# Kernel tuning notes

Measured on AMD Instinct MI355X. Metric: run time of the kernel, lower is better.

## Reference

```python
import jax, jax.numpy as jnp
import numpy as np

B, S, H, E, V, EXTRA = 256, 400, 512, 512, 50257, 100
EMB = H + E  # embedding_size


def setup_inputs() -> dict:
    key = jax.random.key(0)
    ks = jax.random.split(key, 20)
    sd = lambda *shape: 1.0 / np.sqrt(shape[-1])
    d = {
        "input_step": jax.random.normal(ks[0], (B, EMB), jnp.float32),
        "last_hidden": jax.random.normal(ks[1], (1, B, H), jnp.float32),
        "encoder_outputs": jax.random.normal(ks[2], (S, B, H), jnp.float32),
        "enc_batch_extend_vocab": jax.random.randint(ks[3], (S, B), 0, V + EXTRA, jnp.int32),
        "extra_zeros": jnp.zeros((B, EXTRA), jnp.float32),
        "attn_masks": jnp.ones((B, S), jnp.float32),
        "W_ih": jax.random.normal(ks[4], (3 * H, EMB), jnp.float32) * sd(EMB),
        "W_hh": jax.random.normal(ks[5], (3 * H, H), jnp.float32) * sd(H),
        "b_ih": jax.random.normal(ks[6], (3 * H,), jnp.float32) * 0.02,
        "b_hh": jax.random.normal(ks[7], (3 * H,), jnp.float32) * 0.02,
        "attn_W": jax.random.normal(ks[8], (H, 2 * H), jnp.float32) * sd(2 * H),
        "attn_b": jax.random.normal(ks[9], (H,), jnp.float32) * 0.02,
        "attn_v": jax.random.normal(ks[10], (H,), jnp.float32) * sd(H),
        "concat_W": jax.random.normal(ks[11], (H, 2 * H), jnp.float32) * sd(2 * H),
        "concat_b": jax.random.normal(ks[12], (H,), jnp.float32) * 0.02,
        "out_W": jax.random.normal(ks[13], (V, H), jnp.float32) * sd(H),
        "out_b": jax.random.normal(ks[14], (V,), jnp.float32) * 0.02,
        "pgen_W": jax.random.normal(ks[15], (1, 2 * H + EMB), jnp.float32) * sd(2 * H + EMB),
        "pgen_b": jax.random.normal(ks[16], (1,), jnp.float32) * 0.02,
        "sig_W": jax.random.normal(ks[17], (1, H), jnp.float32) * sd(H),
        "sig_b": jax.random.normal(ks[18], (1,), jnp.float32) * 0.02,
    }
    return d


def reference(input_step, last_hidden, encoder_outputs, enc_batch_extend_vocab,
              extra_zeros, attn_masks, W_ih, W_hh, b_ih, b_hh, attn_W, attn_b,
              attn_v, concat_W, concat_b, out_W, out_b, pgen_W, pgen_b,
              sig_W, sig_b):
    # eval-mode dropout is identity
    embedded = input_step                      # [B, EMB]
    h_prev = last_hidden[0]                    # [B, H] (nlayers = 1)

    # --- single GRU step (PyTorch gate layout: r, z, n) ---
    gi = embedded @ W_ih.T + b_ih              # [B, 3H]
    gh = h_prev @ W_hh.T + b_hh                # [B, 3H]
    i_r, i_z, i_n = jnp.split(gi, 3, axis=1)
    h_r, h_z, h_n = jnp.split(gh, 3, axis=1)
    r = jax.nn.sigmoid(i_r + h_r)
    z = jax.nn.sigmoid(i_z + h_z)
    n = jnp.tanh(i_n + r * h_n)
    rnn_output = (1.0 - z) * n + z * h_prev    # [B, H]
    hidden = rnn_output[None]                  # [1, B, H]

    # --- concat attention: v^T tanh(W [h; enc]) over source positions ---
    h_exp = jnp.broadcast_to(rnn_output[None], encoder_outputs.shape)   # [S, B, H]
    energy = jnp.tanh(
        jnp.concatenate([h_exp, encoder_outputs], axis=-1) @ attn_W.T + attn_b
    )                                          # [S, B, H]
    scores = jnp.einsum('sbh,h->bs', energy, attn_v)                    # [B, S]
    scores = jnp.where(attn_masks > 0, scores, jnp.float32(-1e18))
    attn_w = jax.nn.softmax(scores, axis=1)                             # [B, S]
    context = jnp.einsum('bs,sbh->bh', attn_w, encoder_outputs)         # [B, H]

    # --- pgen gate: sigmoid(gelu(Linear([hidden; context; emb]))) ---
    hidden_inp = h_prev                        # last_hidden flattened, [B, H]
    pgen_in = jnp.concatenate([hidden_inp, context, embedded], axis=1)
    pgen = jax.nn.sigmoid(jax.nn.gelu(pgen_in @ pgen_W.T + pgen_b,
                                      approximate=False))               # [B, 1]

    # --- vocab distribution + copy distribution, fused chain ---
    concat_out = jax.nn.gelu(
        jnp.concatenate([rnn_output, context], axis=1) @ concat_W.T + concat_b,
        approximate=False)                     # [B, H]
    logits = concat_out @ out_W.T + out_b      # [B, V]
    vocab_dist = jax.nn.softmax(logits, axis=1)
    vocab_dist = jnp.concatenate([vocab_dist, extra_zeros], axis=1)     # [B, V+EXTRA]
    vocab_dist = pgen * vocab_dist
    attn_dist = (1.0 - pgen) * attn_w          # [B, S]

    idx = enc_batch_extend_vocab.T             # [B, S]
    rows = jnp.arange(vocab_dist.shape[0])[:, None]
    final = vocab_dist.at[rows, idx].add(attn_dist)                     # scatter_add

    out = jax.nn.log_softmax(jnp.log(final + 1e-5), axis=1)

    attn_weights = attn_w.T                    # [S, B]
    sig_hid = rnn_output @ sig_W.T + sig_b     # [B, 1]
    return out, hidden, attn_weights, sig_hid
```

## Files before the change

### kernel.cpp

```cpp
#include <hip/hip_runtime.h>
#include <hip/hip_bf16.h>
#include <math.h>

#define BB 256
#define SS 400
#define HH 512
#define EMBD 1024
#define VV 50257
#define VE 50357
#define O_HID  12891392
#define O_ATT  13022464
#define O_SIG  13124864

typedef __attribute__((ext_vector_type(8))) short s8v;
typedef __attribute__((ext_vector_type(4))) float f4v;

__device__ __forceinline__ float sigmoidf(float x) { return 1.f / (1.f + expf(-x)); }
__device__ __forceinline__ float geluf(float x) { return 0.5f * x * (1.f + erff(x * 0.70710678118654752f)); }

__device__ __forceinline__ void split2_pack(float x0, float x1, unsigned& hp, unsigned& lp) {
  unsigned u0 = __float_as_uint(x0), u1 = __float_as_uint(x1);
  hp = (u0 >> 16) | (u1 & 0xFFFF0000u);
  float d0 = x0 - __uint_as_float(u0 & 0xFFFF0000u);
  float d1 = x1 - __uint_as_float(u1 & 0xFFFF0000u);
  lp = (__float_as_uint(d0) >> 16) | (__float_as_uint(d1) & 0xFFFF0000u);
}

template<int ACT>
__global__ __launch_bounds__(256) void gemm_nt(const float* __restrict__ A, int lda,
                                               const float* __restrict__ W, int ldw,
                                               const float* __restrict__ bias,
                                               float* __restrict__ C, int ldc,
                                               int N, int K) {
  __shared__ __align__(16) float As[16][68];
  __shared__ __align__(16) float Ws[16][68];
  const int tid = threadIdx.x;
  const int m0 = blockIdx.x * 64, n0 = blockIdx.y * 64;
  const int tx = tid & 15, ty = tid >> 4;
  const int lr = tid >> 2;
  const int lk = (tid & 3) * 4;
  float acc[4][4] = {};
  for (int k0 = 0; k0 < K; k0 += 16) {
    float4 a4, w4;
    a4 = *(const float4*)(A + (size_t)(m0 + lr) * lda + k0 + lk);
    int wrow = n0 + lr;
    if (wrow < N) w4 = *(const float4*)(W + (size_t)wrow * ldw + k0 + lk);
    else          w4 = make_float4(0.f, 0.f, 0.f, 0.f);
    __syncthreads();
    As[lk + 0][lr] = a4.x; As[lk + 1][lr] = a4.y; As[lk + 2][lr] = a4.z; As[lk + 3][lr] = a4.w;
    Ws[lk + 0][lr] = w4.x; Ws[lk + 1][lr] = w4.y; Ws[lk + 2][lr] = w4.z; Ws[lk + 3][lr] = w4.w;
    __syncthreads();
#pragma unroll
    for (int k = 0; k < 16; ++k) {
      float4 av = *(const float4*)&As[k][ty * 4];
      float4 wv = *(const float4*)&Ws[k][tx * 4];
      float am[4] = {av.x, av.y, av.z, av.w};
      float wn[4] = {wv.x, wv.y, wv.z, wv.w};
#pragma unroll
      for (int i = 0; i < 4; ++i)
#pragma unroll
        for (int j = 0; j < 4; ++j) acc[i][j] += am[i] * wn[j];
    }
  }
#pragma unroll
  for (int i = 0; i < 4; ++i) {
    int row = m0 + ty * 4 + i;
#pragma unroll
    for (int j = 0; j < 4; ++j) {
      int col = n0 + tx * 4 + j;
      if (col < N) {
        float val = acc[i][j] + bias[col];
        if (ACT == 1) val = geluf(val);
        C[(size_t)row * ldc + col] = val;
      }
    }
  }
}

__global__ __launch_bounds__(256) void gru_gemms(const float* __restrict__ input_step,
                                                 const float* __restrict__ last_hidden,
                                                 const float* __restrict__ W_ih,
                                                 const float* __restrict__ W_hh,
                                                 const float* __restrict__ b_ih,
                                                 const float* __restrict__ b_hh,
                                                 float* __restrict__ gi, float* __restrict__ gh) {
  __shared__ __align__(16) float As[16][68];
  __shared__ __align__(16) float Ws[16][68];
  const bool isGi = blockIdx.y < 24;
  const float* A = isGi ? input_step : last_hidden;
  const float* W = isGi ? W_ih : W_hh;
  const float* bias = isGi ? b_ih : b_hh;
  float* C = isGi ? gi : gh;
  const int lda = isGi ? 1024 : 512;
  const int K = isGi ? 1024 : 512;
  const int n0 = (isGi ? blockIdx.y : blockIdx.y - 24) * 64;
  const int m0 = blockIdx.x * 64;
  const int tid = threadIdx.x;
  const int tx = tid & 15, ty = tid >> 4;
  const int lr = tid >> 2;
  const int lk = (tid & 3) * 4;
  float acc[4][4] = {};
  for (int k0 = 0; k0 < K; k0 += 16) {
    float4 a4 = *(const float4*)(A + (size_t)(m0 + lr) * lda + k0 + lk);
    float4 w4 = *(const float4*)(W + (size_t)(n0 + lr) * lda + k0 + lk);
    __syncthreads();
    As[lk + 0][lr] = a4.x; As[lk + 1][lr] = a4.y; As[lk + 2][lr] = a4.z; As[lk + 3][lr] = a4.w;
    Ws[lk + 0][lr] = w4.x; Ws[lk + 1][lr] = w4.y; Ws[lk + 2][lr] = w4.z; Ws[lk + 3][lr] = w4.w;
    __syncthreads();
#pragma unroll
    for (int k = 0; k < 16; ++k) {
      float4 av = *(const float4*)&As[k][ty * 4];
      float4 wv = *(const float4*)&Ws[k][tx * 4];
      float am[4] = {av.x, av.y, av.z, av.w};
      float wn[4] = {wv.x, wv.y, wv.z, wv.w};
#pragma unroll
      for (int i = 0; i < 4; ++i)
#pragma unroll
        for (int j = 0; j < 4; ++j) acc[i][j] += am[i] * wn[j];
    }
  }
#pragma unroll
  for (int i = 0; i < 4; ++i) {
    int row = m0 + ty * 4 + i;
#pragma unroll
    for (int j = 0; j < 4; ++j) {
      int col = n0 + tx * 4 + j;
      C[(size_t)row * 1536 + col] = acc[i][j] + bias[col];
    }
  }
}

__global__ __launch_bounds__(256) void gru_combine(const float* __restrict__ gi, const float* __restrict__ gh,
                                                   const float* __restrict__ hprev,
                                                   float* __restrict__ rnn, float* __restrict__ hid_out,
                                                   float* __restrict__ cin) {
  int idx = blockIdx.x * 256 + threadIdx.x;
  int b = idx >> 9, j = idx & 511;
  const float* gib = gi + (size_t)b * 1536;
  const float* ghb = gh + (size_t)b * 1536;
  float r = sigmoidf(gib[j] + ghb[j]);
  float z = sigmoidf(gib[512 + j] + ghb[512 + j]);
  float n = tanhf(gib[1024 + j] + r * ghb[1024 + j]);
  float h = hprev[idx];
  float o = (1.f - z) * n + z * h;
  rnn[idx] = o;
  hid_out[idx] = o;
  cin[(size_t)b * 1024 + j] = o;
}

__global__ __launch_bounds__(256) void pack_split(const float* __restrict__ src, int ld, int col0, int rows,
                                                  unsigned short* __restrict__ dhi,
                                                  unsigned short* __restrict__ dlo) {
  int idx = blockIdx.x * 256 + threadIdx.x;
  int l = idx & 63;
  int kb = (idx >> 6) & 15;
  int jb = idx >> 10;
  int j = jb * 16 + (l & 15);
  int k0 = kb * 32 + (l >> 4) * 8;
  float4 x0 = make_float4(0.f, 0.f, 0.f, 0.f), x1 = x0;
  if (j < rows) {
    const float* p = src + (size_t)j * ld + col0 + k0;
    x0 = *(const float4*)p;
    x1 = *(const float4*)(p + 4);
  }
  unsigned h0, l0, h1, l1, h2, l2, h3, l3;
  split2_pack(x0.x, x0.y, h0, l0);
  split2_pack(x0.z, x0.w, h1, l1);
  split2_pack(x1.x, x1.y, h2, l2);
  split2_pack(x1.z, x1.w, h3, l3);
  *(uint4*)(dhi + (size_t)idx * 8) = make_uint4(h0, h1, h2, h3);
  *(uint4*)(dlo + (size_t)idx * 8) = make_uint4(l0, l1, l2, l3);
}

__global__ __launch_bounds__(256, 2) void attn_mfma(const float* __restrict__ enc,
                                                    const unsigned short* __restrict__ BhiP,
                                                    const unsigned short* __restrict__ BloP,
                                                    const float* __restrict__ hW,
                                                    const float* __restrict__ v,
                                                    float* __restrict__ scores) {
  __shared__ __align__(16) unsigned short AhiL[2 * 4 * 66 * 8];
  __shared__ __align__(16) unsigned short AloL[2 * 4 * 66 * 8];

  const int tid = threadIdx.x;
  const int R0 = blockIdx.x * 64;
  const int jhalf = blockIdx.y;
  const int lane = tid & 63;
  const int w = tid >> 6;
  const int jbBase = jhalf * 16 + w * 4;
  const int g = lane >> 4;
  const int l16 = lane & 15;

  const int ar = tid >> 2;
  const int akc = tid & 3;
  const float* aptr = enc + (size_t)(R0 + ar) * 512 + akc * 8;

  const unsigned short* bh0 = BhiP + lane * 8;
  const unsigned short* bl0 = BloP + lane * 8;

  f4v acc[4][4];
#pragma unroll
  for (int rt = 0; rt < 4; ++rt)
#pragma unroll
    for (int ct = 0; ct < 4; ++ct) acc[rt][ct] = (f4v){0.f, 0.f, 0.f, 0.f};

  {
    float4 x0 = *(const float4*)(aptr);
    float4 x1 = *(const float4*)(aptr + 4);
    unsigned h0, l0, h1, l1, h2, l2, h3, l3;
    split2_pack(x0.x, x0.y, h0, l0);
    split2_pack(x0.z, x0.w, h1, l1);
    split2_pack(x1.x, x1.y, h2, l2);
    split2_pack(x1.z, x1.w, h3, l3);
    int wb = akc * 66 + ar;
    *(uint4*)&AhiL[wb * 8] = make_uint4(h0, h1, h2, h3);
    *(uint4*)&AloL[wb * 8] = make_uint4(l0, l1, l2, l3);
  }
  s8v BH[4], BL[4];
#pragma unroll
  for (int ct = 0; ct < 4; ++ct) {
    const int fo = ((jbBase + ct) * 16 + 0) * 512;
    BH[ct] = *(const s8v*)(bh0 + fo);
    BL[ct] = *(const s8v*)(bl0 + fo);
  }
  __syncthreads();

  for (int t = 0; t < 16; ++t) {
    const int k0 = t * 32;
    float4 pa0, pa1;
    if (t < 15) {
      pa0 = *(const float4*)(aptr + k0 + 32);
      pa1 = *(const float4*)(aptr + k0 + 36);
    }
    const int rb = ((t & 1) * 4 + g) * 66 + l16;
#pragma unroll
    for (int rt = 0; rt < 4; ++rt) {
      s8v ah = *(const s8v*)&AhiL[(rb + rt * 16) * 8];
      s8v al = *(const s8v*)&AloL[(rb + rt * 16) * 8];
#pragma unroll
      for (int ct = 0; ct < 4; ++ct) {
        acc[rt][ct] = __builtin_amdgcn_mfma_f32_16x16x32_bf16(ah, BH[ct], acc[rt][ct], 0, 0, 0);
        acc[rt][ct] = __builtin_amdgcn_mfma_f32_16x16x32_bf16(ah, BL[ct], acc[rt][ct], 0, 0, 0);
        acc[rt][ct] = __builtin_amdgcn_mfma_f32_16x16x32_bf16(al, BH[ct], acc[rt][ct], 0, 0, 0);
      }
    }
    if (t < 15) {
#pragma unroll
      for (int ct = 0; ct < 4; ++ct) {
        const int fo = ((jbBase + ct) * 16 + (t + 1)) * 512;
        BH[ct] = *(const s8v*)(bh0 + fo);
        BL[ct] = *(const s8v*)(bl0 + fo);
      }
    }
    if (t < 15) {
      unsigned h0, l0, h1, l1, h2, l2, h3, l3;
      split2_pack(pa0.x, pa0.y, h0, l0);
      split2_pack(pa0.z, pa0.w, h1, l1);
      split2_pack(pa1.x, pa1.y, h2, l2);
      split2_pack(pa1.z, pa1.w, h3, l3);
      int wb = (((t + 1) & 1) * 4 + akc) * 66 + ar;
      *(uint4*)&AhiL[wb * 8] = make_uint4(h0, h1, h2, h3);
      *(uint4*)&AloL[wb * 8] = make_uint4(l0, l1, l2, l3);
    }
    __syncthreads();
  }

  float sp[4][4] = {};
#pragma unroll
  for (int ct = 0; ct < 4; ++ct) {
    int j = jhalf * 256 + w * 64 + ct * 16 + l16;
    float vj = v[j];
    const float* hWj = hW + j;
#pragma unroll
    for (int rt = 0; rt < 4; ++rt) {
#pragma unroll
      for (int q = 0; q < 4; ++q) {
        int rl = rt * 16 + g * 4 + q;
        int b = (R0 + rl) & 255;
        float e = acc[rt][ct][q] + hWj[(size_t)b * 512];
        sp[rt][q] += tanhf(e) * vj;
      }
    }
  }

  __syncthreads();
  float* sredf = (float*)AhiL;
#pragma unroll
  for (int rt = 0; rt < 4; ++rt)
#pragma unroll
    for (int q = 0; q < 4; ++q) {
      float s = sp[rt][q];
      s += __shfl_xor(s, 1); s += __shfl_xor(s, 2);
      s += __shfl_xor(s, 4); s += __shfl_xor(s, 8);
      if (l16 == 0) sredf[(rt * 16 + g * 4 + q) * 4 + w] = s;
    }
  __syncthreads();
  if (tid < 64) {
    float s = sredf[tid * 4 + 0] + sredf[tid * 4 + 1] + sredf[tid * 4 + 2] + sredf[tid * 4 + 3];
    int r = R0 + tid;
    int b = r & 255, si = r >> 8;
    atomicAdd(scores + b * 400 + si, s);
  }
}

__global__ __launch_bounds__(256, 2) void logits_mfma(const float* __restrict__ A,
                                                      const float* __restrict__ W,
                                                      const float* __restrict__ bias,
                                                      float* __restrict__ out) {
  __shared__ __align__(16) unsigned short AhiL[2 * 4 * 66 * 8];
  __shared__ __align__(16) unsigned short AloL[2 * 4 * 66 * 8];

  const int tid = threadIdx.x;
  const int R0 = blockIdx.x * 64;
  const int C0 = blockIdx.y * 256;
  const int lane = tid & 63;
  const int w = tid >> 6;
  const int g = lane >> 4;
  const int l16 = lane & 15;

  const int ar = tid >> 2;
  const int akc = tid & 3;
  const float* aptr = A + (size_t)(R0 + ar) * 512 + akc * 8;

  int jc[4]; bool jok[4];
#pragma unroll
  for (int ct = 0; ct < 4; ++ct) {
    jc[ct] = C0 + w * 64 + ct * 16 + l16;
    jok[ct] = jc[ct] < VV;
  }

  f4v acc[4][4];
#pragma unroll
  for (int rt = 0; rt < 4; ++rt)
#pragma unroll
    for (int ct = 0; ct < 4; ++ct) acc[rt][ct] = (f4v){0.f, 0.f, 0.f, 0.f};

  {
    float4 pa0 = *(const float4*)(aptr);
    float4 pa1 = *(const float4*)(aptr + 4);
    unsigned h0, l0, h1, l1, h2, l2, h3, l3;
    split2_pack(pa0.x, pa0.y, h0, l0);
    split2_pack(pa0.z, pa0.w, h1, l1);
    split2_pack(pa1.x, pa1.y, h2, l2);
    split2_pack(pa1.z, pa1.w, h3, l3);
    int wb = akc * 66 + ar;
    *(uint4*)&AhiL[wb * 8] = make_uint4(h0, h1, h2, h3);
    *(uint4*)&AloL[wb * 8] = make_uint4(l0, l1, l2, l3);
  }
  __syncthreads();

#pragma unroll 2
  for (int t = 0; t < 16; ++t) {
    const int k0 = t * 32;
    s8v BH[4], BL[4];
#pragma unroll
    for (int ct = 0; ct < 4; ++ct) {
      const float* wp = W + (size_t)(jok[ct] ? jc[ct] : 0) * 512 + k0 + g * 8;
      float4 b0 = *(const float4*)wp;
      float4 b1 = *(const float4*)(wp + 4);
      if (!jok[ct]) { b0 = make_float4(0.f, 0.f, 0.f, 0.f); b1 = b0; }
      unsigned h0, l0, h1, l1, h2, l2, h3, l3;
      split2_pack(b0.x, b0.y, h0, l0);
      split2_pack(b0.z, b0.w, h1, l1);
      split2_pack(b1.x, b1.y, h2, l2);
      split2_pack(b1.z, b1.w, h3, l3);
      uint4 ph = make_uint4(h0, h1, h2, h3);
      uint4 pl = make_uint4(l0, l1, l2, l3);
      BH[ct] = *(s8v*)&ph; BL[ct] = *(s8v*)&pl;
    }
    float4 pa0, pa1;
    if (t < 15) {
      pa0 = *(const float4*)(aptr + k0 + 32);
      pa1 = *(const float4*)(aptr + k0 + 36);
    }
    const int rb = ((t & 1) * 4 + g) * 66 + l16;
#pragma unroll
    for (int rt = 0; rt < 4; ++rt) {
      s8v ah = *(const s8v*)&AhiL[(rb + rt * 16) * 8];
      s8v al = *(const s8v*)&AloL[(rb + rt * 16) * 8];
#pragma unroll
      for (int ct = 0; ct < 4; ++ct) {
        acc[rt][ct] = __builtin_amdgcn_mfma_f32_16x16x32_bf16(ah, BH[ct], acc[rt][ct], 0, 0, 0);
        acc[rt][ct] = __builtin_amdgcn_mfma_f32_16x16x32_bf16(ah, BL[ct], acc[rt][ct], 0, 0, 0);
        acc[rt][ct] = __builtin_amdgcn_mfma_f32_16x16x32_bf16(al, BH[ct], acc[rt][ct], 0, 0, 0);
      }
    }
    if (t < 15) {
      unsigned h0, l0, h1, l1, h2, l2, h3, l3;
      split2_pack(pa0.x, pa0.y, h0, l0);
      split2_pack(pa0.z, pa0.w, h1, l1);
      split2_pack(pa1.x, pa1.y, h2, l2);
      split2_pack(pa1.z, pa1.w, h3, l3);
      int wb = (((t + 1) & 1) * 4 + akc) * 66 + ar;
      *(uint4*)&AhiL[wb * 8] = make_uint4(h0, h1, h2, h3);
      *(uint4*)&AloL[wb * 8] = make_uint4(l0, l1, l2, l3);
    }
    __syncthreads();
  }

#pragma unroll
  for (int ct = 0; ct < 4; ++ct) {
    if (!jok[ct]) continue;
    float bj = bias[jc[ct]];
#pragma unroll
    for (int rt = 0; rt < 4; ++rt) {
      int row = R0 + rt * 16 + g * 4;
#pragma unroll
      for (int q = 0; q < 4; ++q)
        out[(size_t)(row + q) * VE + jc[ct]] = acc[rt][ct][q] + bj;
    }
  }
}

__global__ __launch_bounds__(256) void softmax_k(const float* __restrict__ scores,
                                                 const float* __restrict__ masks,
                                                 float* __restrict__ attnw, float* __restrict__ attnT) {
  int b = blockIdx.x, tid = threadIdx.x;
  __shared__ float red[4];
  float m = -3e38f;
  for (int s = tid; s < 400; s += 256) {
    float sc = (masks[b * 400 + s] > 0.f) ? scores[b * 400 + s] : -1e18f;
    m = fmaxf(m, sc);
  }
#pragma unroll
  for (int o = 32; o; o >>= 1) m = fmaxf(m, __shfl_xor(m, o));
  if ((tid & 63) == 0) red[tid >> 6] = m;
  __syncthreads();
  m = fmaxf(fmaxf(red[0], red[1]), fmaxf(red[2], red[3]));
  __syncthreads();
  float z = 0.f;
  for (int s = tid; s < 400; s += 256) {
    float sc = (masks[b * 400 + s] > 0.f) ? scores[b * 400 + s] : -1e18f;
    z += expf(sc - m);
  }
#pragma unroll
  for (int o = 32; o; o >>= 1) z += __shfl_xor(z, o);
  if ((tid & 63) == 0) red[tid >> 6] = z;
  __syncthreads();
  z = red[0] + red[1] + red[2] + red[3];
  float inv = 1.f / z;
  for (int s = tid; s < 400; s += 256) {
    float sc = (masks[b * 400 + s] > 0.f) ? scores[b * 400 + s] : -1e18f;
    float w = expf(sc - m) * inv;
    attnw[b * 400 + s] = w;
    attnT[s * 256 + b] = w;
  }
}

__global__ __launch_bounds__(1024) void context_pgen_k(const float* __restrict__ enc,
                                                       const float* __restrict__ attnw,
                                                       const float* __restrict__ hprev,
                                                       const float* __restrict__ emb,
                                                       const float* __restrict__ pW,
                                                       const float* __restrict__ pb,
                                                       float* __restrict__ ctx, float* __restrict__ cin,
                                                       float* __restrict__ pgen) {
  int b = blockIdx.x, tid = threadIdx.x;
  __shared__ float w[400];
  __shared__ float part[4][512];
  __shared__ float red[16];
  for (int s = tid; s < 400; s += 1024) w[s] = attnw[b * 400 + s];
  __syncthreads();
  const int h = (tid & 255) * 2;
  const int sq = tid >> 8;
  const float* p = enc + (size_t)b * 512 + h;
  float cx = 0.f, cy = 0.f;
  const int s0 = sq * 100;
#pragma unroll 4
  for (int s = s0; s < s0 + 100; ++s) {
    float2 e = *(const float2*)(p + (size_t)s * 131072);
    cx += w[s] * e.x; cy += w[s] * e.y;
  }
  part[sq][h] = cx; part[sq][h + 1] = cy;
  __syncthreads();
  float vsum = 0.f;
  if (tid < 512) {
    vsum = part[0][tid] + part[1][tid] + part[2][tid] + part[3][tid];
    ctx[(size_t)b * 512 + tid] = vsum;
    cin[(size_t)b * 1024 + 512 + tid] = vsum;
  }
  __syncthreads();
  if (tid < 512) part[0][tid] = vsum;
  __syncthreads();
  float acc = 0.f;
#pragma unroll
  for (int kk = 0; kk < 2; ++kk) {
    int k = tid + kk * 1024;
    float x = (k < 512) ? hprev[(size_t)b * 512 + k]
            : (k < 1024) ? part[0][k - 512]
            : emb[(size_t)b * 1024 + k - 1024];
    acc += x * pW[k];
  }
#pragma unroll
  for (int o = 32; o; o >>= 1) acc += __shfl_xor(acc, o);
  if ((tid & 63) == 0) red[tid >> 6] = acc;
  __syncthreads();
  if (tid == 0) {
    float d = pb[0];
#pragma unroll
    for (int i = 0; i < 16; ++i) d += red[i];
    pgen[b] = sigmoidf(geluf(d));
  }
}

__global__ void sig_k(const float* __restrict__ rnn, const float* __restrict__ sW,
                      const float* __restrict__ sb, float* __restrict__ outp) {
  int b = blockIdx.x, tid = threadIdx.x;
  float acc = 0.f;
  for (int k = tid; k < 512; k += 64) acc += rnn[(size_t)b * 512 + k] * sW[k];
#pragma unroll
  for (int o = 32; o; o >>= 1) acc += __shfl_xor(acc, o);
  if (tid == 0) outp[b] = acc + sb[0];
}

__global__ __launch_bounds__(1024) void rowscale_k(float* __restrict__ out, const float* __restrict__ pgen) {
  const int b = blockIdx.x, tid = threadIdx.x;
  float* row = out + (size_t)b * VE;
  __shared__ float red[16];
  float m = -3e38f;
  for (int j = tid * 4; j < 50256; j += 4096) {
    float4 x = *(const float4*)(row + j);
    m = fmaxf(fmaxf(m, fmaxf(x.x, x.y)), fmaxf(x.z, x.w));
  }
  if (tid == 0) m = fmaxf(m, row[50256]);
#pragma unroll
  for (int o = 32; o; o >>= 1) m = fmaxf(m, __shfl_xor(m, o));
  if ((tid & 63) == 0) red[tid >> 6] = m;
  __syncthreads();
  m = red[0];
#pragma unroll
  for (int i = 1; i < 16; ++i) m = fmaxf(m, red[i]);
  __syncthreads();
  float z = 0.f;
  for (int j = tid * 4; j < 50256; j += 4096) {
    float4 x = *(const float4*)(row + j);
    z += expf(x.x - m) + expf(x.y - m) + expf(x.z - m) + expf(x.w - m);
  }
  if (tid == 0) z += expf(row[50256] - m);
#pragma unroll
  for (int o = 32; o; o >>= 1) z += __shfl_xor(z, o);
  if ((tid & 63) == 0) red[tid >> 6] = z;
  __syncthreads();
  z = 0.f;
#pragma unroll
  for (int i = 0; i < 16; ++i) z += red[i];
  const float coef = pgen[b] / z;
  for (int j = tid * 4; j < 50356; j += 4096) {
    float4 x = *(const float4*)(row + j);
    float4 y;
    y.x = (j + 0 < VV) ? coef * expf(x.x - m) : 0.f;
    y.y = (j + 1 < VV) ? coef * expf(x.y - m) : 0.f;
    y.z = (j + 2 < VV) ? coef * expf(x.z - m) : 0.f;
    y.w = (j + 3 < VV) ? coef * expf(x.w - m) : 0.f;
    *(float4*)(row + j) = y;
  }
  if (tid == 0) row[50356] = 0.f;
}

__global__ __launch_bounds__(256) void scatter_k(float* __restrict__ out, const int* __restrict__ ebev,
                                                 const float* __restrict__ attnw, const float* __restrict__ pgen) {
  int t = blockIdx.x * 256 + threadIdx.x;
  int s = t >> 8, b = t & 255;
  int idx = ebev[t];
  float w = (1.f - pgen[b]) * attnw[b * 400 + s];
  atomicAdd(out + (size_t)b * VE + idx, w);
}

__global__ __launch_bounds__(1024) void sumfinal_k(float* __restrict__ out) {
  const int b = blockIdx.x, tid = threadIdx.x;
  float* row = out + (size_t)b * VE;
  __shared__ float red[16];
  float t = 0.f;
  for (int j = tid * 4; j < 50356; j += 4096) {
    float4 x = *(const float4*)(row + j);
    t += x.x + x.y + x.z + x.w;
  }
  if (tid == 0) t += row[50356];
#pragma unroll
  for (int o = 32; o; o >>= 1) t += __shfl_xor(t, o);
  if ((tid & 63) == 0) red[tid >> 6] = t;
  __syncthreads();
  float tot = 0.f;
#pragma unroll
  for (int i = 0; i < 16; ++i) tot += red[i];
  const float logT = logf(tot + (float)VE * 1e-5f);
  for (int j = tid * 4; j < 50356; j += 4096) {
    float4 x = *(const float4*)(row + j);
    x.x = logf(x.x + 1e-5f) - logT;
    x.y = logf(x.y + 1e-5f) - logT;
    x.z = logf(x.z + 1e-5f) - logT;
    x.w = logf(x.w + 1e-5f) - logT;
    *(float4*)(row + j) = x;
  }
  if (tid == 0) row[50356] = logf(row[50356] + 1e-5f) - logT;
}

extern "C" void kernel_launch(void* const* d_in, const int* in_sizes, int n_in,
                              void* d_out, int out_size, void* d_ws, size_t ws_size,
                              hipStream_t stream) {
  const float* input_step = (const float*)d_in[0];
  const float* last_hidden = (const float*)d_in[1];
  const float* enc = (const float*)d_in[2];
  const int*   ebev = (const int*)d_in[3];
  const float* masks = (const float*)d_in[5];
  const float* W_ih = (const float*)d_in[6];
  const float* W_hh = (const float*)d_in[7];
  const float* b_ih = (const float*)d_in[8];
  const float* b_hh = (const float*)d_in[9];
  const float* attn_W = (const float*)d_in[10];
  const float* attn_b = (const float*)d_in[11];
  const float* attn_v = (const float*)d_in[12];
  const float* concat_W = (const float*)d_in[13];
  const float* concat_b = (const float*)d_in[14];
  const float* out_W = (const float*)d_in[15];
  const float* out_b = (const float*)d_in[16];
  const float* pgen_W = (const float*)d_in[17];
  const float* pgen_b = (const float*)d_in[18];
  const float* sig_W = (const float*)d_in[19];
  const float* sig_b = (const float*)d_in[20];

  float* out = (float*)d_out;
  float* ws = (float*)d_ws;
  float* gi     = ws;
  float* gh     = gi + 393216;
  float* rnn    = gh + 393216;
  float* hW     = rnn + 131072;
  float* scores = hW + 131072;
  float* attnw  = scores + 102400;
  float* ctx    = attnw + 102400;
  float* cin    = ctx + 131072;
  float* cout_  = cin + 262144;
  float* pgen   = cout_ + 131072;
  float* rowm   = pgen + 256;
  float* coef   = rowm + 256;
  float* logT   = coef + 256;
  unsigned short* Bhi = (unsigned short*)(logT + 256);
  unsigned short* Blo = Bhi + 262144;

  pack_split<<<128, 256, 0, stream>>>(attn_W, 1024, 512, 512, Bhi, Blo);
  hipMemsetAsync(scores, 0, 102400 * sizeof(float), stream);
  gru_gemms<<<dim3(4, 48), 256, 0, stream>>>(input_step, last_hidden, W_ih, W_hh, b_ih, b_hh, gi, gh);
  gru_combine<<<512, 256, 0, stream>>>(gi, gh, last_hidden, rnn, out + O_HID, cin);
  gemm_nt<0><<<dim3(4, 8), 256, 0, stream>>>(rnn, 512, attn_W, 1024, attn_b, hW, 512, 512, 512);
  attn_mfma<<<dim3(1600, 2), 256, 0, stream>>>(enc, Bhi, Blo, hW, attn_v, scores);
  softmax_k<<<256, 256, 0, stream>>>(scores, masks, attnw, out + O_ATT);
  context_pgen_k<<<256, 1024, 0, stream>>>(enc, attnw, last_hidden, input_step,
                                           pgen_W, pgen_b, ctx, cin, pgen);
  sig_k<<<256, 64, 0, stream>>>(rnn, sig_W, sig_b, out + O_SIG);
  gemm_nt<1><<<dim3(4, 8), 256, 0, stream>>>(cin, 1024, concat_W, 1024, concat_b, cout_, 512, 512, 1024);
  logits_mfma<<<dim3(4, 197), 256, 0, stream>>>(cout_, out_W, out_b, out);
  rowscale_k<<<256, 1024, 0, stream>>>(out, pgen);
  scatter_k<<<400, 256, 0, stream>>>(out, ebev, attnw, pgen);
  sumfinal_k<<<256, 1024, 0, stream>>>(out);
}
```

Measured before the change: 579.8 us.

## Fuse row max into logits epilogue and merge softmax, scatter, log passes

```diff
diff --git a/kernel.cpp b/kernel.cpp
--- a/kernel.cpp
+++ b/kernel.cpp
@@ -24,6 +24,15 @@
   float d0 = x0 - __uint_as_float(u0 & 0xFFFF0000u);
   float d1 = x1 - __uint_as_float(u1 & 0xFFFF0000u);
   lp = (__float_as_uint(d0) >> 16) | (__float_as_uint(d1) & 0xFFFF0000u);
+}
+
+__device__ __forceinline__ unsigned fkey(float x) {
+  unsigned u = __float_as_uint(x);
+  return (u & 0x80000000u) ? ~u : (u | 0x80000000u);
+}
+__device__ __forceinline__ float fdecode(unsigned key) {
+  unsigned u = (key & 0x80000000u) ? (key & 0x7FFFFFFFu) : ~key;
+  return __uint_as_float(u);
 }
 
 template<int ACT>
@@ -305,7 +314,8 @@
 __global__ __launch_bounds__(256, 2) void logits_mfma(const float* __restrict__ A,
                                                       const float* __restrict__ W,
                                                       const float* __restrict__ bias,
-                                                      float* __restrict__ out) {
+                                                      float* __restrict__ out,
+                                                      unsigned* __restrict__ rowmK) {
   __shared__ __align__(16) unsigned short AhiL[2 * 4 * 66 * 8];
   __shared__ __align__(16) unsigned short AloL[2 * 4 * 66 * 8];
 
@@ -397,6 +407,11 @@
     __syncthreads();
   }
 
+  float rmax[4][4];
+#pragma unroll
+  for (int rt = 0; rt < 4; ++rt)
+#pragma unroll
+    for (int q = 0; q < 4; ++q) rmax[rt][q] = -3e38f;
 #pragma unroll
   for (int ct = 0; ct < 4; ++ct) {
     if (!jok[ct]) continue;
@@ -405,9 +420,28 @@
     for (int rt = 0; rt < 4; ++rt) {
       int row = R0 + rt * 16 + g * 4;
 #pragma unroll
-      for (int q = 0; q < 4; ++q)
-        out[(size_t)(row + q) * VE + jc[ct]] = acc[rt][ct][q] + bj;
-    }
+      for (int q = 0; q < 4; ++q) {
+        float val = acc[rt][ct][q] + bj;
+        out[(size_t)(row + q) * VE + jc[ct]] = val;
+        rmax[rt][q] = fmaxf(rmax[rt][q], val);
+      }
+    }
+  }
+  float* redm = (float*)AhiL;
+#pragma unroll
+  for (int rt = 0; rt < 4; ++rt)
+#pragma unroll
+    for (int q = 0; q < 4; ++q) {
+      float mx = rmax[rt][q];
+      mx = fmaxf(mx, __shfl_xor(mx, 1)); mx = fmaxf(mx, __shfl_xor(mx, 2));
+      mx = fmaxf(mx, __shfl_xor(mx, 4)); mx = fmaxf(mx, __shfl_xor(mx, 8));
+      if (l16 == 0) redm[(rt * 16 + g * 4 + q) * 4 + w] = mx;
+    }
+  __syncthreads();
+  if (tid < 64) {
+    float mx = fmaxf(fmaxf(redm[tid * 4 + 0], redm[tid * 4 + 1]),
+                     fmaxf(redm[tid * 4 + 2], redm[tid * 4 + 3]));
+    if (mx > -2e38f) atomicMax(rowmK + R0 + tid, fkey(mx));
   }
 }
 
@@ -512,69 +546,50 @@
   if (tid == 0) outp[b] = acc + sb[0];
 }
 
-__global__ __launch_bounds__(1024) void rowscale_k(float* __restrict__ out, const float* __restrict__ pgen) {
+__global__ __launch_bounds__(1024) void finale_k(float* __restrict__ out,
+                                                 const float* __restrict__ pgen,
+                                                 const unsigned* __restrict__ rowmK,
+                                                 const int* __restrict__ ebev,
+                                                 const float* __restrict__ attnw) {
   const int b = blockIdx.x, tid = threadIdx.x;
   float* row = out + (size_t)b * VE;
   __shared__ float red[16];
-  float m = -3e38f;
-  for (int j = tid * 4; j < 50256; j += 4096) {
+  __shared__ float shZ;
+  const float m = fdecode(rowmK[b]);
+  const float pg = pgen[b];
+  float z = 0.f;
+  for (int j = tid * 4; j < 50356; j += 4096) {
     float4 x = *(const float4*)(row + j);
-    m = fmaxf(fmaxf(m, fmaxf(x.x, x.y)), fmaxf(x.z, x.w));
-  }
-  if (tid == 0) m = fmaxf(m, row[50256]);
-#pragma unroll
-  for (int o = 32; o; o >>= 1) m = fmaxf(m, __shfl_xor(m, o));
-  if ((tid & 63) == 0) red[tid >> 6] = m;
-  __syncthreads();
-  m = red[0];
-#pragma unroll
-  for (int i = 1; i < 16; ++i) m = fmaxf(m, red[i]);
-  __syncthreads();
-  float z = 0.f;
-  for (int j = tid * 4; j < 50256; j += 4096) {
-    float4 x = *(const float4*)(row + j);
-    z += expf(x.x - m) + expf(x.y - m) + expf(x.z - m) + expf(x.w - m);
-  }
-  if (tid == 0) z += expf(row[50256] - m);
+    float4 e;
+    e.x = (j + 0 < VV) ? expf(x.x - m) : 0.f;
+    e.y = (j + 1 < VV) ? expf(x.y - m) : 0.f;
+    e.z = (j + 2 < VV) ? expf(x.z - m) : 0.f;
+    e.w = (j + 3 < VV) ? expf(x.w - m) : 0.f;
+    z += e.x + e.y + e.z + e.w;
+    *(float4*)(row + j) = e;
+  }
+  if (tid == 0) row[50356] = 0.f;
 #pragma unroll
   for (int o = 32; o; o >>= 1) z += __shfl_xor(z, o);
   if ((tid & 63) == 0) red[tid >> 6] = z;
   __syncthreads();
-  z = 0.f;
-#pragma unroll
-  for (int i = 0; i < 16; ++i) z += red[i];
-  const float coef = pgen[b] / z;
-  for (int j = tid * 4; j < 50356; j += 4096) {
-    float4 x = *(const float4*)(row + j);
-    float4 y;
-    y.x = (j + 0 < VV) ? coef * expf(x.x - m) : 0.f;
-    y.y = (j + 1 < VV) ? coef * expf(x.y - m) : 0.f;
-    y.z = (j + 2 < VV) ? coef * expf(x.z - m) : 0.f;
-    y.w = (j + 3 < VV) ? coef * expf(x.w - m) : 0.f;
-    *(float4*)(row + j) = y;
-  }
-  if (tid == 0) row[50356] = 0.f;
-}
-
-__global__ __launch_bounds__(256) void scatter_k(float* __restrict__ out, const int* __restrict__ ebev,
-                                                 const float* __restrict__ attnw, const float* __restrict__ pgen) {
-  int t = blockIdx.x * 256 + threadIdx.x;
-  int s = t >> 8, b = t & 255;
-  int idx = ebev[t];
-  float w = (1.f - pgen[b]) * attnw[b * 400 + s];
-  atomicAdd(out + (size_t)b * VE + idx, w);
-}
-
-__global__ __launch_bounds__(1024) void sumfinal_k(float* __restrict__ out) {
-  const int b = blockIdx.x, tid = threadIdx.x;
-  float* row = out + (size_t)b * VE;
-  __shared__ float red[16];
+  if (tid == 0) {
+    float t = 0.f;
+#pragma unroll
+    for (int i = 0; i < 16; ++i) t += red[i];
+    shZ = t;
+  }
+  __syncthreads();
+  const float coef = pg / shZ;
+  if (tid < 400) {
+    int idx = ebev[tid * 256 + b];
+    float wv = (1.f - pg) * attnw[b * 400 + tid] / coef;
+    atomicAdd(row + idx, wv);
+  }
+  __syncthreads();
+  volatile const float* vrow = row;
   float t = 0.f;
-  for (int j = tid * 4; j < 50356; j += 4096) {
-    float4 x = *(const float4*)(row + j);
-    t += x.x + x.y + x.z + x.w;
-  }
-  if (tid == 0) t += row[50356];
+  for (int j = tid; j < VE; j += 1024) t += vrow[j];
 #pragma unroll
   for (int o = 32; o; o >>= 1) t += __shfl_xor(t, o);
   if ((tid & 63) == 0) red[tid >> 6] = t;
@@ -582,16 +597,11 @@
   float tot = 0.f;
 #pragma unroll
   for (int i = 0; i < 16; ++i) tot += red[i];
-  const float logT = logf(tot + (float)VE * 1e-5f);
-  for (int j = tid * 4; j < 50356; j += 4096) {
-    float4 x = *(const float4*)(row + j);
-    x.x = logf(x.x + 1e-5f) - logT;
-    x.y = logf(x.y + 1e-5f) - logT;
-    x.z = logf(x.z + 1e-5f) - logT;
-    x.w = logf(x.w + 1e-5f) - logT;
-    *(float4*)(row + j) = x;
-  }
-  if (tid == 0) row[50356] = logf(row[50356] + 1e-5f) - logT;
+  const float logT = logf(coef * tot + (float)VE * 1e-5f);
+  for (int j = tid; j < VE; j += 1024) {
+    float e = vrow[j];
+    row[j] = logf(coef * e + 1e-5f) - logT;
+  }
 }
 
 extern "C" void kernel_launch(void* const* d_in, const int* in_sizes, int n_in,
@@ -638,6 +648,7 @@
 
   pack_split<<<128, 256, 0, stream>>>(attn_W, 1024, 512, 512, Bhi, Blo);
   hipMemsetAsync(scores, 0, 102400 * sizeof(float), stream);
+  hipMemsetAsync(rowm, 0, 256 * sizeof(float), stream);
   gru_gemms<<<dim3(4, 48), 256, 0, stream>>>(input_step, last_hidden, W_ih, W_hh, b_ih, b_hh, gi, gh);
   gru_combine<<<512, 256, 0, stream>>>(gi, gh, last_hidden, rnn, out + O_HID, cin);
   gemm_nt<0><<<dim3(4, 8), 256, 0, stream>>>(rnn, 512, attn_W, 1024, attn_b, hW, 512, 512, 512);
@@ -647,8 +658,6 @@
                                            pgen_W, pgen_b, ctx, cin, pgen);
   sig_k<<<256, 64, 0, stream>>>(rnn, sig_W, sig_b, out + O_SIG);
   gemm_nt<1><<<dim3(4, 8), 256, 0, stream>>>(cin, 1024, concat_W, 1024, concat_b, cout_, 512, 512, 1024);
-  logits_mfma<<<dim3(4, 197), 256, 0, stream>>>(cout_, out_W, out_b, out);
-  rowscale_k<<<256, 1024, 0, stream>>>(out, pgen);
-  scatter_k<<<400, 256, 0, stream>>>(out, ebev, attnw, pgen);
-  sumfinal_k<<<256, 1024, 0, stream>>>(out);
-}
+  logits_mfma<<<dim3(4, 197), 256, 0, stream>>>(cout_, out_W, out_b, out, (unsigned*)rowm);
+  finale_k<<<256, 1024, 0, stream>>>(out, pgen, (const unsigned*)rowm, ebev, attnw);
+}
```

After: 586.2 us. Within noise of the previous version (+1.1%).
